# Kernel optimization log

Measured on AMD Instinct MI355X. Metric: run time of the kernel, lower is better.

## Reference

```python
import jax, jax.numpy as jnp
import numpy as np

B, T, C, H = 8, 1024, 768, 12
HD = C // H  # 64


def setup_inputs() -> dict:
    key = jax.random.key(0)
    ks = jax.random.split(key, 9)
    s = 0.02
    x = jax.random.normal(ks[0], (B, T, C), dtype=jnp.float32)
    mask = jnp.tril(jnp.ones((T, T), dtype=bool))[None, None, :, :]  # causal [1,1,T,T]
    wq = jax.random.normal(ks[1], (C, C), dtype=jnp.float32) * s
    wk = jax.random.normal(ks[2], (C, C), dtype=jnp.float32) * s
    wv = jax.random.normal(ks[3], (C, C), dtype=jnp.float32) * s
    wo = jax.random.normal(ks[4], (C, C), dtype=jnp.float32) * s
    bq = jnp.zeros((C,), dtype=jnp.float32)
    bk = jnp.zeros((C,), dtype=jnp.float32)
    bv = jnp.zeros((C,), dtype=jnp.float32)
    bo = jnp.zeros((C,), dtype=jnp.float32)
    return {"x": x, "mask": mask, "wq": wq, "bq": bq, "wk": wk, "bk": bk,
            "wv": wv, "bv": bv, "wo": wo, "bo": bo}


def reference(x, mask, wq, bq, wk, bk, wv, bv, wo, bo):
    Bx, Tx, Cx = x.shape
    # QKV projections (flax Dense: y = x @ W + b)
    q = (x @ wq + bq).reshape(Bx, Tx, H, HD).transpose(0, 2, 1, 3)  # [B,H,T,hd]
    k = (x @ wk + bk).reshape(Bx, Tx, H, HD).transpose(0, 2, 1, 3)
    v = (x @ wv + bv).reshape(Bx, Tx, H, HD).transpose(0, 2, 1, 3)
    attn = jnp.einsum('bhtd,bhsd->bhts', q, k) / jnp.sqrt(jnp.float32(HD))
    attn = jnp.where(mask, attn, jnp.float32(-1e9))
    attn = jax.nn.softmax(attn, axis=-1)
    out = jnp.einsum('bhts,bhsd->bhtd', attn, v)  # [B,H,T,hd]
    out = out.transpose(0, 2, 1, 3).reshape(Bx, Tx, Cx)
    return out @ wo + bo
```

## Files before the change

### kernel.cpp

```cpp
#include <hip/hip_runtime.h>
#include <hip/hip_bf16.h>

typedef __bf16 bf16_t;
typedef __bf16 bf16x8 __attribute__((ext_vector_type(8)));
typedef float f32x4 __attribute__((ext_vector_type(4)));

#define NB 8
#define NT 1024
#define NC 768
#define NH 12
#define NHD 64

__device__ __forceinline__ f32x4 mfma16(bf16x8 a, bf16x8 b, f32x4 c) {
  return __builtin_amdgcn_mfma_f32_16x16x32_bf16(a, b, c, 0, 0, 0);
}

__device__ __forceinline__ void gld_lds16(const void* g, void* l) {
  __builtin_amdgcn_global_load_lds((const __attribute__((address_space(1))) void*)g,
                                   (__attribute__((address_space(3))) void*)l, 16, 0, 0);
}

__global__ void cvt_x(const float* __restrict__ in, bf16_t* __restrict__ out, int n4) {
  int i = blockIdx.x * blockDim.x + threadIdx.x;
  if (i >= n4) return;
  float4 v = ((const float4*)in)[i];
  bf16_t o[4] = {(bf16_t)v.x, (bf16_t)v.y, (bf16_t)v.z, (bf16_t)v.w};
  *(uint2*)(out + i * 4) = *(uint2*)o;
}

__global__ void transpose_w(const float* __restrict__ wq, const float* __restrict__ wk,
                            const float* __restrict__ wv, const float* __restrict__ wo,
                            bf16_t* __restrict__ wqkvT, bf16_t* __restrict__ woT) {
  __shared__ float tile[32][33];
  const int m = blockIdx.z;
  const float* in = (m == 0) ? wq : (m == 1) ? wk : (m == 2) ? wv : wo;
  bf16_t* out = (m == 3) ? woT : (wqkvT + m * NC * NC);
  const int tx = threadIdx.x & 31, ty = threadIdx.x >> 5;
  const int x = blockIdx.x * 32 + tx;
  const int y0 = blockIdx.y * 32;
#pragma unroll
  for (int i = 0; i < 32; i += 8)
    tile[ty + i][tx] = in[(size_t)(y0 + ty + i) * NC + x];
  __syncthreads();
  const int ox = y0 + tx;
  const int oy0 = blockIdx.x * 32;
#pragma unroll
  for (int i = 0; i < 32; i += 8)
    out[(size_t)(oy0 + ty + i) * NC + ox] = (bf16_t)tile[tx][ty + i];
}

__global__ void transpose_v(const bf16_t* __restrict__ V, bf16_t* __restrict__ VT) {
  __shared__ bf16_t tile[32][33];
  const int bh = blockIdx.z;
  const int x0 = blockIdx.x * 32;
  const int y0 = blockIdx.y * 32;
  const int tx = threadIdx.x & 31, ty = threadIdx.x >> 5;
  const bf16_t* in = V + (size_t)bh * NT * NHD;
  bf16_t* out = VT + (size_t)bh * NHD * NT;
#pragma unroll
  for (int i = 0; i < 32; i += 8)
    tile[ty + i][tx] = in[(size_t)(y0 + ty + i) * NHD + x0 + tx];
  __syncthreads();
#pragma unroll
  for (int i = 0; i < 32; i += 8)
    out[(size_t)(x0 + ty + i) * NT + y0 + tx] = tile[tx][ty + i];
}

template <int MODE, int BM>
__global__ __launch_bounds__(256) void gemm_t(
    const bf16_t* __restrict__ A, const bf16_t* __restrict__ BT, int K,
    const float* __restrict__ b0, const float* __restrict__ b1,
    const float* __restrict__ b2, float* __restrict__ outF,
    bf16_t* __restrict__ out0, bf16_t* __restrict__ out1,
    bf16_t* __restrict__ out2) {
  constexpr int NJ = (BM == 128) ? 4 : 2;
  __shared__ __align__(16) bf16_t lA[BM * 32];
  __shared__ __align__(16) bf16_t lB[128 * 32];
  const int tid = threadIdx.x;
  const int lane = tid & 63, wave = tid >> 6;
  const int quad = lane >> 4, l16 = lane & 15;
  const int bm = blockIdx.x * BM, bn = blockIdx.y * 128;
  const int wm = (BM == 128) ? (wave >> 1) * 64 : 0;
  const int wn = (BM == 128) ? (wave & 1) * 64 : wave * 32;

  const int ra = tid >> 2;
  const int cc = tid & 3;
  const int kca = cc ^ ((ra >> 1) & 3);

  f32x4 acc[4][NJ] = {};
  char* lAb = (char*)lA;
  char* lBb = (char*)lB;

  for (int k0 = 0; k0 < K; k0 += 32) {
    __syncthreads();
    gld_lds16(A + (size_t)(bm + ra) * K + k0 + kca * 8, lAb + wave * 1024);
    if (BM == 128)
      gld_lds16(A + (size_t)(bm + 64 + ra) * K + k0 + kca * 8, lAb + 4096 + wave * 1024);
    gld_lds16(BT + (size_t)(bn + ra) * K + k0 + kca * 8, lBb + wave * 1024);
    gld_lds16(BT + (size_t)(bn + 64 + ra) * K + k0 + kca * 8, lBb + 4096 + wave * 1024);
    __syncthreads();

    bf16x8 af[4], bfr[NJ];
#pragma unroll
    for (int i = 0; i < 4; i++) {
      int row = wm + i * 16 + l16;
      int ch = quad ^ ((row >> 1) & 3);
      af[i] = *(const bf16x8*)(lAb + row * 64 + ch * 16);
    }
#pragma unroll
    for (int j = 0; j < NJ; j++) {
      int row = wn + j * 16 + l16;
      int ch = quad ^ ((row >> 1) & 3);
      bfr[j] = *(const bf16x8*)(lBb + row * 64 + ch * 16);
    }
#pragma unroll
    for (int i = 0; i < 4; i++)
#pragma unroll
      for (int j = 0; j < NJ; j++)
        acc[i][j] = mfma16(af[i], bfr[j], acc[i][j]);
  }

  if (MODE == 0) {
#pragma unroll
    for (int j = 0; j < NJ; j++) {
      int n = bn + wn + j * 16 + l16;
      float bias = b0[n];
#pragma unroll
      for (int i = 0; i < 4; i++) {
        int m0 = bm + wm + i * 16 + quad * 4;
#pragma unroll
        for (int r = 0; r < 4; r++)
          outF[(size_t)(m0 + r) * NC + n] = acc[i][j][r] + bias;
      }
    }
  } else {
#pragma unroll
    for (int j = 0; j < NJ; j++) {
      int n = bn + wn + j * 16 + l16;
      int sel = n / 768;
      int nl = n - sel * 768;
      int h = nl >> 6, d = nl & 63;
      const float* bp = (sel == 0) ? b0 : (sel == 1) ? b1 : b2;
      bf16_t* dst = (sel == 0) ? out0 : (sel == 1) ? out1 : out2;
      float bias = bp[nl];
      float scl = (sel == 0) ? 0.125f : 1.0f;
#pragma unroll
      for (int i = 0; i < 4; i++) {
        int m0 = bm + wm + i * 16 + quad * 4;
#pragma unroll
        for (int r = 0; r < 4; r++) {
          int m = m0 + r;
          int bb = m >> 10, t = m & 1023;
          dst[((size_t)(bb * NH + h) * NT + t) * NHD + d] =
              (bf16_t)((acc[i][j][r] + bias) * scl);
        }
      }
    }
  }
}

__global__ __launch_bounds__(256) void attn_fwd(
    const bf16_t* __restrict__ Q, const bf16_t* __restrict__ Kt,
    const bf16_t* __restrict__ VT, bf16_t* __restrict__ AO) {
  __shared__ __align__(16) bf16_t lK[64 * 72];
  __shared__ __align__(16) bf16_t lV[64 * 72];
  __shared__ __align__(16) bf16_t lP[8][16 * 72];
  const int tid = threadIdx.x, lane = tid & 63, wave = tid >> 6;
  const int quad = lane >> 4, l16 = lane & 15;
  const int bh = blockIdx.x;
  const int bx = blockIdx.y;
  const int b = bh / NH, h = bh - b * NH;
  const int qtA = bx, qtB = 15 - bx;
  const int jmax = qtB;

  const size_t qbase = (size_t)bh * NT;
  const size_t qoffA = (qbase + qtA * 64 + wave * 16 + l16) * NHD;
  const size_t qoffB = (qbase + qtB * 64 + wave * 16 + l16) * NHD;
  const bf16x8 aqA0 = *(const bf16x8*)(Q + qoffA + quad * 8);
  const bf16x8 aqA1 = *(const bf16x8*)(Q + qoffA + 32 + quad * 8);
  const bf16x8 aqB0 = *(const bf16x8*)(Q + qoffB + quad * 8);
  const bf16x8 aqB1 = *(const bf16x8*)(Q + qoffB + 32 + quad * 8);

  f32x4 lsA = {0.f, 0.f, 0.f, 0.f}, lsB = lsA;
  f32x4 OfA[4] = {}, OfB[4] = {};
  const f32x4 zero = {0.f, 0.f, 0.f, 0.f};

  const int r0 = tid >> 3, p0 = tid & 7;
  const bf16_t* Kg0 = Kt + qbase * NHD;
  const bf16_t* Vg0 = VT + (size_t)bh * 64 * NT;

  uint4 gk0 = *(const uint4*)(Kg0 + (size_t)r0 * 64 + p0 * 8);
  uint4 gk1 = *(const uint4*)(Kg0 + (size_t)(r0 + 32) * 64 + p0 * 8);
  uint4 gv0 = *(const uint4*)(Vg0 + (size_t)r0 * NT + p0 * 8);
  uint4 gv1 = *(const uint4*)(Vg0 + (size_t)(r0 + 32) * NT + p0 * 8);

  bf16_t* lPA = lP[wave * 2 + 0];
  bf16_t* lPB = lP[wave * 2 + 1];
  const int sb = quad ^ (l16 >> 2);

  for (int j = 0; j <= jmax; ++j) {
    __syncthreads();
    *(uint4*)(lK + r0 * 72 + p0 * 8) = gk0;
    *(uint4*)(lK + (r0 + 32) * 72 + p0 * 8) = gk1;
    *(uint4*)(lV + r0 * 72 + p0 * 8) = gv0;
    *(uint4*)(lV + (r0 + 32) * 72 + p0 * 8) = gv1;
    __syncthreads();
    if (j < jmax) {
      const bf16_t* Kg = Kg0 + (size_t)(j + 1) * 64 * NHD;
      const bf16_t* Vg = Vg0 + (j + 1) * 64;
      gk0 = *(const uint4*)(Kg + (size_t)r0 * 64 + p0 * 8);
      gk1 = *(const uint4*)(Kg + (size_t)(r0 + 32) * 64 + p0 * 8);
      gv0 = *(const uint4*)(Vg + (size_t)r0 * NT + p0 * 8);
      gv1 = *(const uint4*)(Vg + (size_t)(r0 + 32) * NT + p0 * 8);
    }
    const bool actA = (j <= qtA);

    f32x4 sA[4], sB[4];
#pragma unroll
    for (int nn = 0; nn < 4; nn++) {
      int row = nn * 16 + l16;
      bf16x8 k0 = *(const bf16x8*)(lK + row * 72 + quad * 8);
      bf16x8 k1 = *(const bf16x8*)(lK + row * 72 + 32 + quad * 8);
      sB[nn] = mfma16(aqB0, k0, zero);
      sB[nn] = mfma16(aqB1, k1, sB[nn]);
      if (actA) {
        sA[nn] = mfma16(aqA0, k0, zero);
        sA[nn] = mfma16(aqA1, k1, sA[nn]);
      }
    }

    if (j == qtB) {
#pragma unroll
      for (int nn = 0; nn < 4; nn++) {
        int key = nn * 16 + l16;
#pragma unroll
        for (int r = 0; r < 4; r++) {
          int qrow = wave * 16 + quad * 4 + r;
          if (key > qrow) sB[nn][r] = -1e30f;
        }
      }
    }
    if (actA && j == qtA) {
#pragma unroll
      for (int nn = 0; nn < 4; nn++) {
        int key = nn * 16 + l16;
#pragma unroll
        for (int r = 0; r < 4; r++) {
          int qrow = wave * 16 + quad * 4 + r;
          if (key > qrow) sA[nn][r] = -1e30f;
        }
      }
    }

#pragma unroll
    for (int nn = 0; nn < 4; nn++)
#pragma unroll
      for (int r = 0; r < 4; r++) {
        float pv = __expf(sB[nn][r]);
        lsB[r] += pv;
        lPB[(quad * 4 + r) * 72 + ((nn * 16 + l16) ^ (quad * 8))] = (bf16_t)pv;
      }
    if (actA) {
#pragma unroll
      for (int nn = 0; nn < 4; nn++)
#pragma unroll
        for (int r = 0; r < 4; r++) {
          float pv = __expf(sA[nn][r]);
          lsA[r] += pv;
          lPA[(quad * 4 + r) * 72 + ((nn * 16 + l16) ^ (quad * 8))] = (bf16_t)pv;
        }
    }
    asm volatile("s_waitcnt lgkmcnt(0)" ::: "memory");

    const bf16x8 apB0 = *(const bf16x8*)(lPB + l16 * 72 + sb * 8);
    const bf16x8 apB1 = *(const bf16x8*)(lPB + l16 * 72 + (sb + 4) * 8);
    bf16x8 apA0, apA1;
    if (actA) {
      apA0 = *(const bf16x8*)(lPA + l16 * 72 + sb * 8);
      apA1 = *(const bf16x8*)(lPA + l16 * 72 + (sb + 4) * 8);
    }
#pragma unroll
    for (int dd = 0; dd < 4; dd++) {
      int row = dd * 16 + l16;
      bf16x8 v0 = *(const bf16x8*)(lV + row * 72 + quad * 8);
      bf16x8 v1 = *(const bf16x8*)(lV + row * 72 + 32 + quad * 8);
      OfB[dd] = mfma16(apB0, v0, OfB[dd]);
      OfB[dd] = mfma16(apB1, v1, OfB[dd]);
      if (actA) {
        OfA[dd] = mfma16(apA0, v0, OfA[dd]);
        OfA[dd] = mfma16(apA1, v1, OfA[dd]);
      }
    }
  }

#pragma unroll
  for (int off = 8; off >= 1; off >>= 1)
#pragma unroll
    for (int r = 0; r < 4; r++) {
      lsA[r] += __shfl_xor(lsA[r], off, 64);
      lsB[r] += __shfl_xor(lsB[r], off, 64);
    }

#pragma unroll
  for (int g = 0; g < 2; g++) {
    f32x4* Of = g ? OfB : OfA;
    f32x4& lrun = g ? lsB : lsA;
    const int qt = g ? qtB : qtA;
    f32x4 inv;
#pragma unroll
    for (int r = 0; r < 4; r++) inv[r] = 1.0f / lrun[r];
    const int tq = qt * 64 + wave * 16 + quad * 4;
#pragma unroll
    for (int dd = 0; dd < 4; dd++) {
      int col = h * 64 + dd * 16 + l16;
#pragma unroll
      for (int r = 0; r < 4; r++)
        AO[((size_t)b * NT + tq + r) * NC + col] = (bf16_t)(Of[dd][r] * inv[r]);
    }
  }
}

extern "C" void kernel_launch(void* const* d_in, const int* in_sizes, int n_in,
                              void* d_out, int out_size, void* d_ws, size_t ws_size,
                              hipStream_t stream) {
  const float* x = (const float*)d_in[0];
  const float* wq = (const float*)d_in[2];
  const float* bq = (const float*)d_in[3];
  const float* wk = (const float*)d_in[4];
  const float* bk = (const float*)d_in[5];
  const float* wv = (const float*)d_in[6];
  const float* bv = (const float*)d_in[7];
  const float* wo = (const float*)d_in[8];
  const float* bo = (const float*)d_in[9];

  float* outF = (float*)d_out;
  bf16_t* Qb = (bf16_t*)d_out;
  bf16_t* Vb = Qb + (size_t)NB * NH * NT * NHD;
  bf16_t* ws = (bf16_t*)d_ws;
  bf16_t* xb = ws;
  bf16_t* wqkvT = xb + (size_t)NB * NT * NC;
  bf16_t* woT = wqkvT + (size_t)2304 * 768;
  bf16_t* Kb = woT + (size_t)768 * 768;
  bf16_t* VTb = Kb + (size_t)NB * NH * NT * NHD;
  bf16_t* AO = VTb + (size_t)NB * NH * NT * NHD;

  const int n4 = NB * NT * NC / 4;
  cvt_x<<<(n4 + 255) / 256, 256, 0, stream>>>(x, xb, n4);
  transpose_w<<<dim3(24, 24, 4), 256, 0, stream>>>(wq, wk, wv, wo, wqkvT, woT);
  gemm_t<1, 128><<<dim3(64, 18), 256, 0, stream>>>(xb, wqkvT, NC, bq, bk, bv,
                                                   nullptr, Qb, Kb, Vb);
  transpose_v<<<dim3(2, 32, 96), 256, 0, stream>>>(Vb, VTb);
  attn_fwd<<<dim3(96, 8), 256, 0, stream>>>(Qb, Kb, VTb, AO);
  gemm_t<0, 64><<<dim3(128, 6), 256, 0, stream>>>(AO, woT, NC, bo, nullptr, nullptr,
                                                  outF, nullptr, nullptr, nullptr);
}
```

Baseline: 211.3 us.

## Double-buffer attention K/V via direct-to-LDS loads and vectorize GEMM epilogue stores

The attention kernel now double-buffers K and V tiles in LDS. It issues global_load_lds for the next tile straight into an XOR-swizzled buffer, replacing the register staging and its extra barrier. The GEMM swaps the MFMA operand order so each lane holds four consecutive output columns. That allows float4 and packed bf16x4 stores with vectorized bias loads instead of scalar strided writes. The risks are correctness of the async load waits given a single barrier per iteration, and the larger LDS footprint.

```diff
diff --git a/kernel.cpp b/kernel.cpp
--- a/kernel.cpp
+++ b/kernel.cpp
@@ -87,7 +87,7 @@
   const int cc = tid & 3;
   const int kca = cc ^ ((ra >> 1) & 3);
 
-  f32x4 acc[4][NJ] = {};
+  f32x4 acc[NJ][4] = {};
   char* lAb = (char*)lA;
   char* lBb = (char*)lB;
 
@@ -114,46 +114,50 @@
       bfr[j] = *(const bf16x8*)(lBb + row * 64 + ch * 16);
     }
 #pragma unroll
-    for (int i = 0; i < 4; i++)
-#pragma unroll
-      for (int j = 0; j < NJ; j++)
-        acc[i][j] = mfma16(af[i], bfr[j], acc[i][j]);
+    for (int j = 0; j < NJ; j++)
+#pragma unroll
+      for (int i = 0; i < 4; i++)
+        acc[j][i] = mfma16(bfr[j], af[i], acc[j][i]);
   }
 
   if (MODE == 0) {
 #pragma unroll
     for (int j = 0; j < NJ; j++) {
-      int n = bn + wn + j * 16 + l16;
-      float bias = b0[n];
+      int n0 = bn + wn + j * 16 + quad * 4;
+      float4 b4 = *(const float4*)(b0 + n0);
+      float bb4[4] = {b4.x, b4.y, b4.z, b4.w};
 #pragma unroll
       for (int i = 0; i < 4; i++) {
-        int m0 = bm + wm + i * 16 + quad * 4;
-#pragma unroll
-        for (int r = 0; r < 4; r++)
-          outF[(size_t)(m0 + r) * NC + n] = acc[i][j][r] + bias;
+        int m = bm + wm + i * 16 + l16;
+        float4 o;
+        o.x = acc[j][i][0] + bb4[0];
+        o.y = acc[j][i][1] + bb4[1];
+        o.z = acc[j][i][2] + bb4[2];
+        o.w = acc[j][i][3] + bb4[3];
+        *(float4*)(outF + (size_t)m * NC + n0) = o;
       }
     }
   } else {
 #pragma unroll
     for (int j = 0; j < NJ; j++) {
-      int n = bn + wn + j * 16 + l16;
-      int sel = n / 768;
-      int nl = n - sel * 768;
-      int h = nl >> 6, d = nl & 63;
+      int n0 = bn + wn + j * 16 + quad * 4;
+      int sel = n0 / 768;
+      int nl = n0 - sel * 768;
+      int h = nl >> 6, d0 = nl & 63;
       const float* bp = (sel == 0) ? b0 : (sel == 1) ? b1 : b2;
       bf16_t* dst = (sel == 0) ? out0 : (sel == 1) ? out1 : out2;
-      float bias = bp[nl];
+      float4 b4 = *(const float4*)(bp + nl);
+      float bb4[4] = {b4.x, b4.y, b4.z, b4.w};
       float scl = (sel == 0) ? 0.125f : 1.0f;
 #pragma unroll
       for (int i = 0; i < 4; i++) {
-        int m0 = bm + wm + i * 16 + quad * 4;
-#pragma unroll
-        for (int r = 0; r < 4; r++) {
-          int m = m0 + r;
-          int bb = m >> 10, t = m & 1023;
-          dst[((size_t)(bb * NH + h) * NT + t) * NHD + d] =
-              (bf16_t)((acc[i][j][r] + bias) * scl);
-        }
+        int m = bm + wm + i * 16 + l16;
+        int bb = m >> 10, t = m & 1023;
+        bf16_t o[4];
+#pragma unroll
+        for (int r = 0; r < 4; r++)
+          o[r] = (bf16_t)((acc[j][i][r] + bb4[r]) * scl);
+        *(uint2*)(dst + ((size_t)(bb * NH + h) * NT + t) * NHD + d0) = *(uint2*)o;
       }
     }
   }
@@ -162,8 +166,8 @@
 __global__ __launch_bounds__(256) void attn_fwd(
     const bf16_t* __restrict__ Q, const bf16_t* __restrict__ Kt,
     const bf16_t* __restrict__ VT, bf16_t* __restrict__ AO) {
-  __shared__ __align__(16) bf16_t lK[64 * 72];
-  __shared__ __align__(16) bf16_t lV[64 * 72];
+  __shared__ __align__(16) bf16_t lK[2][64 * 64];
+  __shared__ __align__(16) bf16_t lV[2][64 * 64];
   __shared__ __align__(16) bf16_t lP[8][16 * 72];
   const int tid = threadIdx.x, lane = tid & 63, wave = tid >> 6;
   const int quad = lane >> 4, l16 = lane & 15;
@@ -185,42 +189,46 @@
   f32x4 OfA[4] = {}, OfB[4] = {};
   const f32x4 zero = {0.f, 0.f, 0.f, 0.f};
 
-  const int r0 = tid >> 3, p0 = tid & 7;
+  const int sr = tid >> 3;
+  const int sc = (tid & 7) ^ (sr & 7);
   const bf16_t* Kg0 = Kt + qbase * NHD;
   const bf16_t* Vg0 = VT + (size_t)bh * 64 * NT;
-
-  uint4 gk0 = *(const uint4*)(Kg0 + (size_t)r0 * 64 + p0 * 8);
-  uint4 gk1 = *(const uint4*)(Kg0 + (size_t)(r0 + 32) * 64 + p0 * 8);
-  uint4 gv0 = *(const uint4*)(Vg0 + (size_t)r0 * NT + p0 * 8);
-  uint4 gv1 = *(const uint4*)(Vg0 + (size_t)(r0 + 32) * NT + p0 * 8);
+  const size_t kO0 = (size_t)sr * 64 + sc * 8, kO1 = kO0 + (size_t)32 * 64;
+  const size_t vO0 = (size_t)sr * NT + sc * 8, vO1 = vO0 + (size_t)32 * NT;
 
   bf16_t* lPA = lP[wave * 2 + 0];
   bf16_t* lPB = lP[wave * 2 + 1];
   const int sb = quad ^ (l16 >> 2);
 
+#define STAGE(JT, BUF)                                                  \
+  do {                                                                  \
+    const bf16_t* Kg_ = Kg0 + (size_t)(JT) * 64 * NHD;                  \
+    const bf16_t* Vg_ = Vg0 + (JT) * 64;                                \
+    char* dK_ = (char*)lK[BUF] + wave * 1024;                           \
+    char* dV_ = (char*)lV[BUF] + wave * 1024;                           \
+    gld_lds16(Kg_ + kO0, dK_);                                          \
+    gld_lds16(Kg_ + kO1, dK_ + 4096);                                   \
+    gld_lds16(Vg_ + vO0, dV_);                                          \
+    gld_lds16(Vg_ + vO1, dV_ + 4096);                                   \
+  } while (0)
+
+  STAGE(0, 0);
+
   for (int j = 0; j <= jmax; ++j) {
+    const int cur = j & 1;
     __syncthreads();
-    *(uint4*)(lK + r0 * 72 + p0 * 8) = gk0;
-    *(uint4*)(lK + (r0 + 32) * 72 + p0 * 8) = gk1;
-    *(uint4*)(lV + r0 * 72 + p0 * 8) = gv0;
-    *(uint4*)(lV + (r0 + 32) * 72 + p0 * 8) = gv1;
-    __syncthreads();
-    if (j < jmax) {
-      const bf16_t* Kg = Kg0 + (size_t)(j + 1) * 64 * NHD;
-      const bf16_t* Vg = Vg0 + (j + 1) * 64;
-      gk0 = *(const uint4*)(Kg + (size_t)r0 * 64 + p0 * 8);
-      gk1 = *(const uint4*)(Kg + (size_t)(r0 + 32) * 64 + p0 * 8);
-      gv0 = *(const uint4*)(Vg + (size_t)r0 * NT + p0 * 8);
-      gv1 = *(const uint4*)(Vg + (size_t)(r0 + 32) * NT + p0 * 8);
-    }
+    if (j < jmax) STAGE(j + 1, cur ^ 1);
+    const bf16_t* lKc = lK[cur];
+    const bf16_t* lVc = lV[cur];
     const bool actA = (j <= qtA);
 
     f32x4 sA[4], sB[4];
 #pragma unroll
     for (int nn = 0; nn < 4; nn++) {
       int row = nn * 16 + l16;
-      bf16x8 k0 = *(const bf16x8*)(lK + row * 72 + quad * 8);
-      bf16x8 k1 = *(const bf16x8*)(lK + row * 72 + 32 + quad * 8);
+      int sw = row & 7;
+      bf16x8 k0 = *(const bf16x8*)((char*)lKc + row * 128 + (quad ^ sw) * 16);
+      bf16x8 k1 = *(const bf16x8*)((char*)lKc + row * 128 + ((quad + 4) ^ sw) * 16);
       sB[nn] = mfma16(aqB0, k0, zero);
       sB[nn] = mfma16(aqB1, k1, sB[nn]);
       if (actA) {
@@ -282,8 +290,9 @@
 #pragma unroll
     for (int dd = 0; dd < 4; dd++) {
       int row = dd * 16 + l16;
-      bf16x8 v0 = *(const bf16x8*)(lV + row * 72 + quad * 8);
-      bf16x8 v1 = *(const bf16x8*)(lV + row * 72 + 32 + quad * 8);
+      int sw = row & 7;
+      bf16x8 v0 = *(const bf16x8*)((char*)lVc + row * 128 + (quad ^ sw) * 16);
+      bf16x8 v1 = *(const bf16x8*)((char*)lVc + row * 128 + ((quad + 4) ^ sw) * 16);
       OfB[dd] = mfma16(apB0, v0, OfB[dd]);
       OfB[dd] = mfma16(apB1, v1, OfB[dd]);
       if (actA) {
@@ -292,6 +301,7 @@
       }
     }
   }
+#undef STAGE
 
 #pragma unroll
   for (int off = 8; off >= 1; off >>= 1)
```

New measurement: 209.5 us. No clear change (-0.8%).
